# Kernel tuning notes

Measured on AMD Instinct MI355X. Metric: run time of the kernel, lower is better.

The kernel has to match this reference:

```python
import jax, jax.numpy as jnp
import numpy as np

N_NODES, N_EDGES = 50000, 800000
N_IN, E_IN, N_OUT, E_OUT = 64, 32, 64, 32


def _xavier(key, fan_in, fan_out):
    std = (2.0 / (fan_in + fan_out)) ** 0.5
    return jax.random.normal(key, (fan_in, fan_out), dtype=jnp.float32) * std


def setup_inputs() -> dict:
    key = jax.random.key(0)
    ks = jax.random.split(key, 10)
    return {
        "feat": jax.random.normal(ks[0], (N_NODES, N_IN), dtype=jnp.float32),
        "edge_feat": jax.random.normal(ks[1], (N_EDGES, E_IN), dtype=jnp.float32),
        "w_msg": _xavier(ks[2], N_IN + E_IN, N_OUT),
        "b_msg": jnp.zeros((N_OUT,), dtype=jnp.float32),
        "w_node": _xavier(ks[3], N_IN + N_OUT, N_OUT),
        "b_node": jnp.zeros((N_OUT,), dtype=jnp.float32),
        "w_edge": _xavier(ks[4], N_IN + N_OUT + E_IN, E_OUT),
        "b_edge": jnp.zeros((E_OUT,), dtype=jnp.float32),
        "src_idx": jax.random.randint(ks[5], (N_EDGES,), 0, N_NODES, dtype=jnp.int32),
        "dst_idx": jax.random.randint(ks[6], (N_EDGES,), 0, N_NODES, dtype=jnp.int32),
    }


def reference(feat, edge_feat, w_msg, b_msg, w_node, b_node, w_edge, b_edge, src_idx, dst_idx):
    n_nodes = feat.shape[0]
    # --- message: gather src + edge, linear, tanh --- [E, n_out]
    src_h = feat[src_idx]
    m = jnp.tanh(jnp.concatenate([src_h, edge_feat], axis=1) @ w_msg + b_msg)
    # --- scatter-mean into destination nodes --- [N, n_out]
    sums = jax.ops.segment_sum(m, dst_idx, num_segments=n_nodes)
    cnt = jax.ops.segment_sum(jnp.ones((m.shape[0], 1), m.dtype), dst_idx, num_segments=n_nodes)
    neigh = sums / jnp.maximum(cnt, 1.0)
    # --- node update: cat([neigh, h]) -> linear -> tanh (dropout = identity in eval) ---
    h = jnp.tanh(jnp.concatenate([neigh, feat], axis=1) @ w_node + b_node)
    # --- edge update: cat([src h, dst neigh(updated), edge h]) -> linear -> tanh ---
    e = jnp.tanh(jnp.concatenate([src_h, h[dst_idx], edge_feat], axis=1) @ w_edge + b_edge)
    return h, e
```

## Files before the change

### kernel.cpp

```cpp
#include <hip/hip_runtime.h>

#define NNODES 50000
#define NEDGES 800000
#define NPAD   50176
#define NTILE_E (NEDGES / 16)
#define NTILE_N (NNODES / 16)

typedef __attribute__((ext_vector_type(8))) short bf16x8;
typedef __attribute__((ext_vector_type(4))) float f32x4;

union ABu { bf16x8 v; uint4 u; };

__device__ __forceinline__ float fast_tanh(float x) {
    float e = __expf(2.0f * x);
    return 1.0f - 2.0f * __builtin_amdgcn_rcpf(e + 1.0f);
}

__device__ __forceinline__ unsigned pk_rne(float x, float y) {
    unsigned a = __float_as_uint(x), b = __float_as_uint(y);
    a = (a + 0x7fffu + ((a >> 16) & 1u)) >> 16;
    b = (b + 0x7fffu + ((b >> 16) & 1u)) >> 16;
    return a | (b << 16);
}
__device__ __forceinline__ unsigned pk_tr(float a, float b) {
    return __builtin_amdgcn_perm(__float_as_uint(b), __float_as_uint(a), 0x07060302);
}
__device__ __forceinline__ float bf16_lo(unsigned u) { return __uint_as_float(u << 16); }
__device__ __forceinline__ float bf16_hi(unsigned u) { return __uint_as_float(u & 0xffff0000u); }

__device__ __forceinline__ ABu make_afrag(const float* p) {
    float4 a = ((const float4*)p)[0];
    float4 b = ((const float4*)p)[1];
    ABu r;
    r.u.x = pk_tr(a.x, a.y); r.u.y = pk_tr(a.z, a.w);
    r.u.z = pk_tr(b.x, b.y); r.u.w = pk_tr(b.z, b.w);
    return r;
}

template <int LDN>
__device__ __forceinline__ ABu make_bfrag_u(const unsigned* wp) {
    ABu r;
    r.u.x = wp[0 * LDN]; r.u.y = wp[1 * LDN];
    r.u.z = wp[2 * LDN]; r.u.w = wp[3 * LDN];
    return r;
}

template <int KH, int N>
__device__ __forceinline__ void stage_w(const float* __restrict__ w, unsigned* wl_u) {
    for (int i = threadIdx.x; i < KH * N; i += 256) {
        const int kp = i / N, n = i % N;
        wl_u[i] = pk_rne(w[(2 * kp) * N + n], w[(2 * kp + 1) * N + n]);
    }
}

#define MFMA(a, b, c) __builtin_amdgcn_mfma_f32_16x16x32_bf16((a).v, (b).v, (c), 0, 0, 0)

__global__ __launch_bounds__(256) void hist_kernel(const int* __restrict__ dst_idx,
                                                   int* __restrict__ cnt,
                                                   int* __restrict__ rank) {
    const int base = (blockIdx.x * 256 + threadIdx.x) * 4;
    if (base + 4 <= NEDGES) {
        int4 d = *(const int4*)(dst_idx + base);
        int4 r;
        r.x = atomicAdd(&cnt[d.x], 1);
        r.y = atomicAdd(&cnt[d.y], 1);
        r.z = atomicAdd(&cnt[d.z], 1);
        r.w = atomicAdd(&cnt[d.w], 1);
        *(int4*)(rank + base) = r;
    }
}

__global__ __launch_bounds__(256) void scan1(const int* __restrict__ cnt,
                                             int* __restrict__ off,
                                             int* __restrict__ btot) {
    __shared__ int s[256];
    const int tid = threadIdx.x;
    const int g = blockIdx.x * 256 + tid;
    const int own = cnt[g];
    s[tid] = own;
    __syncthreads();
    for (int o = 1; o < 256; o <<= 1) {
        int v = (tid >= o) ? s[tid - o] : 0;
        __syncthreads();
        s[tid] += v;
        __syncthreads();
    }
    off[g] = s[tid] - own;
    if (tid == 255) btot[blockIdx.x] = s[255];
}

__global__ __launch_bounds__(256) void scan3b(int* __restrict__ off,
                                              const int* __restrict__ btot) {
    __shared__ int s[256];
    const int tid = threadIdx.x;
    s[tid] = btot[tid];
    __syncthreads();
    for (int o = 1; o < 256; o <<= 1) {
        int v = (tid >= o) ? s[tid - o] : 0;
        __syncthreads();
        s[tid] += v;
        __syncthreads();
    }
    const int add = (blockIdx.x == 0) ? 0 : s[blockIdx.x - 1];
    off[blockIdx.x * 256 + tid] += add;
}

__global__ __launch_bounds__(256) void rows_kernel(const int* __restrict__ dst_idx,
                                                   const int* __restrict__ off,
                                                   int* __restrict__ rank) {
    const int base = (blockIdx.x * 256 + threadIdx.x) * 4;
    if (base + 4 <= NEDGES) {
        int4 d = *(const int4*)(dst_idx + base);
        int4 r = *(const int4*)(rank + base);
        r.x += off[d.x];
        r.y += off[d.y];
        r.z += off[d.z];
        r.w += off[d.w];
        *(int4*)(rank + base) = r;
    }
}

__global__ __launch_bounds__(256) void proj2_kernel(
    const float* __restrict__ feat,
    const float* __restrict__ w_m, const float* __restrict__ b_m,
    const float* __restrict__ w_e, const float* __restrict__ b_e,
    float* __restrict__ projm, float* __restrict__ p1) {
    __shared__ __align__(16) unsigned wlm[32 * 64];
    __shared__ __align__(16) unsigned wle[32 * 32];
    stage_w<32, 64>(w_m, wlm);
    stage_w<32, 32>(w_e, wle);
    __syncthreads();

    const int lane = threadIdx.x & 63, wave = threadIdx.x >> 6;
    const int col = lane & 15, quad = lane >> 4;

    ABu bfm[2][4], bfe[2][2];
#pragma unroll
    for (int kc = 0; kc < 2; ++kc) {
#pragma unroll
        for (int nt = 0; nt < 4; ++nt)
            bfm[kc][nt] = make_bfrag_u<64>(&wlm[(kc * 16 + (quad << 2)) * 64 + nt * 16 + col]);
#pragma unroll
        for (int nt = 0; nt < 2; ++nt)
            bfe[kc][nt] = make_bfrag_u<32>(&wle[(kc * 16 + (quad << 2)) * 32 + nt * 16 + col]);
    }

    float bim[4], bie[2];
#pragma unroll
    for (int nt = 0; nt < 4; ++nt) bim[nt] = b_m[nt * 16 + col];
#pragma unroll
    for (int nt = 0; nt < 2; ++nt) bie[nt] = b_e[nt * 16 + col];

    const int nw = gridDim.x << 2;
    for (int t = (blockIdx.x << 2) + wave; t < NTILE_N; t += nw) {
        const int n0 = t << 4;
        const int n = n0 + col;
        ABu a0 = make_afrag(feat + (size_t)n * 64 + (quad << 3));
        ABu a1 = make_afrag(feat + (size_t)n * 64 + 32 + (quad << 3));

        f32x4 accm[4], acce[2];
#pragma unroll
        for (int nt = 0; nt < 4; ++nt)
            accm[nt] = (f32x4){bim[nt], bim[nt], bim[nt], bim[nt]};
#pragma unroll
        for (int nt = 0; nt < 2; ++nt)
            acce[nt] = (f32x4){bie[nt], bie[nt], bie[nt], bie[nt]};
#pragma unroll
        for (int nt = 0; nt < 4; ++nt) {
            accm[nt] = MFMA(a0, bfm[0][nt], accm[nt]);
            accm[nt] = MFMA(a1, bfm[1][nt], accm[nt]);
        }
#pragma unroll
        for (int nt = 0; nt < 2; ++nt) {
            acce[nt] = MFMA(a0, bfe[0][nt], acce[nt]);
            acce[nt] = MFMA(a1, bfe[1][nt], acce[nt]);
        }
#pragma unroll
        for (int i = 0; i < 4; ++i) {
            const int nr = n0 + (quad << 2) + i;
            float4 om = {accm[0][i], accm[1][i], accm[2][i], accm[3][i]};
            *(float4*)(projm + (size_t)nr * 64 + (col << 2)) = om;
            float2 oe = {acce[0][i], acce[1][i]};
            *(float2*)(p1 + (size_t)nr * 32 + (col << 1)) = oe;
        }
    }
}

struct MsgBuf { ABu a2; float4 f4[4]; int4 rows; };

__device__ __forceinline__ void msg_load(
    int t, int col, int quad,
    const float* __restrict__ edge_feat, const float* __restrict__ projm,
    const int* __restrict__ src_idx, const int* __restrict__ rows, MsgBuf& b) {
    const int e0 = t << 4;
    const int4 s4 = *(const int4*)(src_idx + e0 + (quad << 2));
    b.rows = *(const int4*)(rows + e0 + (quad << 2));
    b.a2 = make_afrag(edge_feat + (size_t)(e0 + col) * 32 + (quad << 3));
    b.f4[0] = *(const float4*)(projm + (size_t)s4.x * 64 + (col << 2));
    b.f4[1] = *(const float4*)(projm + (size_t)s4.y * 64 + (col << 2));
    b.f4[2] = *(const float4*)(projm + (size_t)s4.z * 64 + (col << 2));
    b.f4[3] = *(const float4*)(projm + (size_t)s4.w * 64 + (col << 2));
}

__device__ __forceinline__ void msg_comp(
    int col, const ABu (&bf)[4], const MsgBuf& b, unsigned* __restrict__ m_out) {
    f32x4 acc[4];
#pragma unroll
    for (int nt = 0; nt < 4; ++nt) acc[nt] = (f32x4){0.f, 0.f, 0.f, 0.f};
#pragma unroll
    for (int nt = 0; nt < 4; ++nt) acc[nt] = MFMA(b.a2, bf[nt], acc[nt]);
    const int rw[4] = {b.rows.x, b.rows.y, b.rows.z, b.rows.w};
#pragma unroll
    for (int i = 0; i < 4; ++i) {
        uint2 o;
        o.x = pk_rne(fast_tanh(acc[0][i] + b.f4[i].x), fast_tanh(acc[1][i] + b.f4[i].y));
        o.y = pk_rne(fast_tanh(acc[2][i] + b.f4[i].z), fast_tanh(acc[3][i] + b.f4[i].w));
        *(uint2*)(m_out + (size_t)rw[i] * 32 + (col << 1)) = o;
    }
}

__global__ __launch_bounds__(256) void msg_kernel(
    const float* __restrict__ edge_feat, const float* __restrict__ w_bot,
    const int* __restrict__ src_idx, const int* __restrict__ rows,
    const float* __restrict__ projm, unsigned* __restrict__ m_out) {
    __shared__ __align__(16) unsigned wl[16 * 64];
    stage_w<16, 64>(w_bot, wl);
    __syncthreads();

    const int lane = threadIdx.x & 63, wave = threadIdx.x >> 6;
    const int col = lane & 15, quad = lane >> 4;

    ABu bf[4];
#pragma unroll
    for (int nt = 0; nt < 4; ++nt)
        bf[nt] = make_bfrag_u<64>(&wl[(quad << 2) * 64 + nt * 16 + col]);

    const int nw = gridDim.x << 2;
    int t = (blockIdx.x << 2) + wave;
    if (t >= NTILE_E) return;
    MsgBuf A, B;
    msg_load(t, col, quad, edge_feat, projm, src_idx, rows, A);
    for (;;) {
        const int t2 = t + nw;
        if (t2 < NTILE_E)
            msg_load(t2, col, quad, edge_feat, projm, src_idx, rows, B);
        msg_comp(col, bf, A, m_out);
        if (t2 >= NTILE_E) return;
        const int t3 = t2 + nw;
        if (t3 < NTILE_E)
            msg_load(t3, col, quad, edge_feat, projm, src_idx, rows, A);
        msg_comp(col, bf, B, m_out);
        if (t3 >= NTILE_E) return;
        t = t3;
    }
}

__device__ __forceinline__ int mapk(int ks) {
    return ks < 64 ? ((ks >> 2) + ((ks >> 1) & 1) * 32 + (ks & 1) * 16) : ks;
}

__global__ __launch_bounds__(256) void gnode_kernel(
    const float* __restrict__ feat, const unsigned* __restrict__ m,
    const int* __restrict__ off, const int* __restrict__ cnt,
    const float* __restrict__ w_node, const float* __restrict__ b_node,
    const float* __restrict__ w2,
    float* __restrict__ h, float* __restrict__ p2) {
    __shared__ __align__(16) unsigned wl[64 * 64];
    __shared__ __align__(16) unsigned wl2[32 * 32];
    __shared__ float tr[4][16 * 68];

    for (int i = threadIdx.x; i < 64 * 64; i += 256) {
        const int kp = i >> 6, n = i & 63;
        wl[i] = pk_rne(w_node[mapk(2 * kp) * 64 + n], w_node[mapk(2 * kp + 1) * 64 + n]);
    }
    stage_w<32, 32>(w2, wl2);
    __syncthreads();

    const int lane = threadIdx.x & 63, wave = threadIdx.x >> 6;
    const int col = lane & 15, quad = lane >> 4;

    int t = blockIdx.x * 4 + wave;
    if (t > NTILE_N - 1) t = NTILE_N - 1;
    const int n0 = t << 4;
    const int n = n0 + col;
    const int c = cnt[n];
    const int o = off[n];

    float s0[8], s1[8];
#pragma unroll
    for (int j = 0; j < 8; ++j) { s0[j] = 0.f; s1[j] = 0.f; }
    for (int r = 0; r < c; ++r) {
        const unsigned* rp = m + (size_t)(o + r) * 32;
        const uint4 u0 = *(const uint4*)(rp + (quad << 2));
        const uint4 u1 = *(const uint4*)(rp + 16 + (quad << 2));
        s0[0] += bf16_lo(u0.x); s0[1] += bf16_hi(u0.x);
        s0[2] += bf16_lo(u0.y); s0[3] += bf16_hi(u0.y);
        s0[4] += bf16_lo(u0.z); s0[5] += bf16_hi(u0.z);
        s0[6] += bf16_lo(u0.w); s0[7] += bf16_hi(u0.w);
        s1[0] += bf16_lo(u1.x); s1[1] += bf16_hi(u1.x);
        s1[2] += bf16_lo(u1.y); s1[3] += bf16_hi(u1.y);
        s1[4] += bf16_lo(u1.z); s1[5] += bf16_hi(u1.z);
        s1[6] += bf16_lo(u1.w); s1[7] += bf16_hi(u1.w);
    }
    const float inv = __builtin_amdgcn_rcpf((float)max(c, 1));
    ABu a0, a1;
    a0.u.x = pk_tr(s0[0] * inv, s0[1] * inv); a0.u.y = pk_tr(s0[2] * inv, s0[3] * inv);
    a0.u.z = pk_tr(s0[4] * inv, s0[5] * inv); a0.u.w = pk_tr(s0[6] * inv, s0[7] * inv);
    a1.u.x = pk_tr(s1[0] * inv, s1[1] * inv); a1.u.y = pk_tr(s1[2] * inv, s1[3] * inv);
    a1.u.z = pk_tr(s1[4] * inv, s1[5] * inv); a1.u.w = pk_tr(s1[6] * inv, s1[7] * inv);
    const ABu a2 = make_afrag(feat + (size_t)n * 64 + (quad << 3));
    const ABu a3 = make_afrag(feat + (size_t)n * 64 + 32 + (quad << 3));

    f32x4 acc[4];
#pragma unroll
    for (int nt = 0; nt < 4; ++nt) {
        const float bi = b_node[nt * 16 + col];
        acc[nt] = (f32x4){bi, bi, bi, bi};
    }
#pragma unroll
    for (int nt = 0; nt < 4; ++nt) {
        acc[nt] = MFMA(a0, make_bfrag_u<64>(&wl[((quad << 2)) * 64 + nt * 16 + col]), acc[nt]);
        acc[nt] = MFMA(a1, make_bfrag_u<64>(&wl[(16 + (quad << 2)) * 64 + nt * 16 + col]), acc[nt]);
        acc[nt] = MFMA(a2, make_bfrag_u<64>(&wl[(32 + (quad << 2)) * 64 + nt * 16 + col]), acc[nt]);
        acc[nt] = MFMA(a3, make_bfrag_u<64>(&wl[(48 + (quad << 2)) * 64 + nt * 16 + col]), acc[nt]);
    }

    float* trw = tr[wave];
#pragma unroll
    for (int i = 0; i < 4; ++i) {
        const int nr = n0 + (quad << 2) + i;
#pragma unroll
        for (int nt = 0; nt < 4; ++nt) {
            const float ht = fast_tanh(acc[nt][i]);
            h[(size_t)nr * 64 + nt * 16 + col] = ht;
            trw[((quad << 2) + i) * 68 + nt * 16 + col] = ht;
        }
    }
    __syncthreads();

    float f[8], g[8];
#pragma unroll
    for (int j = 0; j < 8; ++j) {
        f[j] = trw[col * 68 + (quad << 3) + j];
        g[j] = trw[col * 68 + 32 + (quad << 3) + j];
    }
    ABu aT0, aT1;
    aT0.u.x = pk_tr(f[0], f[1]); aT0.u.y = pk_tr(f[2], f[3]);
    aT0.u.z = pk_tr(f[4], f[5]); aT0.u.w = pk_tr(f[6], f[7]);
    aT1.u.x = pk_tr(g[0], g[1]); aT1.u.y = pk_tr(g[2], g[3]);
    aT1.u.z = pk_tr(g[4], g[5]); aT1.u.w = pk_tr(g[6], g[7]);

    f32x4 acc2[2];
#pragma unroll
    for (int nt = 0; nt < 2; ++nt) acc2[nt] = (f32x4){0.f, 0.f, 0.f, 0.f};
#pragma unroll
    for (int nt = 0; nt < 2; ++nt) {
        acc2[nt] = MFMA(aT0, make_bfrag_u<32>(&wl2[((quad << 2)) * 32 + nt * 16 + col]), acc2[nt]);
        acc2[nt] = MFMA(aT1, make_bfrag_u<32>(&wl2[(16 + (quad << 2)) * 32 + nt * 16 + col]), acc2[nt]);
    }
#pragma unroll
    for (int i = 0; i < 4; ++i) {
        const int nr = n0 + (quad << 2) + i;
        float2 o2 = {acc2[0][i], acc2[1][i]};
        *(float2*)(p2 + (size_t)nr * 32 + (col << 1)) = o2;
    }
}

struct EBuf { ABu a4; float2 g1[4]; float2 g2[4]; };

__device__ __forceinline__ void edge_load(
    int t, int col, int quad,
    const float* __restrict__ edge_feat,
    const float* __restrict__ p1, const float* __restrict__ p2,
    const int* __restrict__ src_idx, const int* __restrict__ dst_idx, EBuf& b) {
    const int e0 = t << 4;
    const int4 s4 = *(const int4*)(src_idx + e0 + (quad << 2));
    const int4 d4 = *(const int4*)(dst_idx + e0 + (quad << 2));
    b.a4 = make_afrag(edge_feat + (size_t)(e0 + col) * 32 + (quad << 3));
    b.g1[0] = *(const float2*)(p1 + (size_t)s4.x * 32 + (col << 1));
    b.g1[1] = *(const float2*)(p1 + (size_t)s4.y * 32 + (col << 1));
    b.g1[2] = *(const float2*)(p1 + (size_t)s4.z * 32 + (col << 1));
    b.g1[3] = *(const float2*)(p1 + (size_t)s4.w * 32 + (col << 1));
    b.g2[0] = *(const float2*)(p2 + (size_t)d4.x * 32 + (col << 1));
    b.g2[1] = *(const float2*)(p2 + (size_t)d4.y * 32 + (col << 1));
    b.g2[2] = *(const float2*)(p2 + (size_t)d4.z * 32 + (col << 1));
    b.g2[3] = *(const float2*)(p2 + (size_t)d4.w * 32 + (col << 1));
}

__device__ __forceinline__ void edge_comp(
    int t, int col, int quad, const ABu (&bf)[2],
    const EBuf& b, float* __restrict__ e_out) {
    f32x4 acc[2];
#pragma unroll
    for (int nt = 0; nt < 2; ++nt) acc[nt] = (f32x4){0.f, 0.f, 0.f, 0.f};
#pragma unroll
    for (int nt = 0; nt < 2; ++nt) acc[nt] = MFMA(b.a4, bf[nt], acc[nt]);
    const int e0 = t << 4;
#pragma unroll
    for (int i = 0; i < 4; ++i) {
        const int er = e0 + (quad << 2) + i;
        e_out[(size_t)er * 32 + col] = fast_tanh(acc[0][i] + b.g1[i].x + b.g2[i].x);
        e_out[(size_t)er * 32 + 16 + col] = fast_tanh(acc[1][i] + b.g1[i].y + b.g2[i].y);
    }
}

__global__ __launch_bounds__(256) void edge_update(
    const float* __restrict__ edge_feat, const float* __restrict__ w3,
    const float* __restrict__ p1, const float* __restrict__ p2,
    const int* __restrict__ src_idx, const int* __restrict__ dst_idx,
    float* __restrict__ e_out) {
    __shared__ __align__(16) unsigned wl[16 * 32];
    stage_w<16, 32>(w3, wl);
    __syncthreads();

    const int lane = threadIdx.x & 63, wave = threadIdx.x >> 6;
    const int col = lane & 15, quad = lane >> 4;

    ABu bf[2];
#pragma unroll
    for (int nt = 0; nt < 2; ++nt)
        bf[nt] = make_bfrag_u<32>(&wl[(quad << 2) * 32 + nt * 16 + col]);

    const int nw = gridDim.x << 2;
    int t = (blockIdx.x << 2) + wave;
    if (t >= NTILE_E) return;
    EBuf A, B;
    edge_load(t, col, quad, edge_feat, p1, p2, src_idx, dst_idx, A);
    for (;;) {
        const int t2 = t + nw;
        if (t2 < NTILE_E)
            edge_load(t2, col, quad, edge_feat, p1, p2, src_idx, dst_idx, B);
        edge_comp(t, col, quad, bf, A, e_out);
        if (t2 >= NTILE_E) return;
        const int t3 = t2 + nw;
        if (t3 < NTILE_E)
            edge_load(t3, col, quad, edge_feat, p1, p2, src_idx, dst_idx, A);
        edge_comp(t2, col, quad, bf, B, e_out);
        if (t3 >= NTILE_E) return;
        t = t3;
    }
}

extern "C" void kernel_launch(void* const* d_in, const int* in_sizes, int n_in,
                              void* d_out, int out_size, void* d_ws, size_t ws_size,
                              hipStream_t stream) {
    const float* feat      = (const float*)d_in[0];
    const float* edge_feat = (const float*)d_in[1];
    const float* w_msg     = (const float*)d_in[2];
    const float* b_msg     = (const float*)d_in[3];
    const float* w_node    = (const float*)d_in[4];
    const float* b_node    = (const float*)d_in[5];
    const float* w_edge    = (const float*)d_in[6];
    const float* b_edge    = (const float*)d_in[7];
    const int*   src_idx   = (const int*)d_in[8];
    const int*   dst_idx   = (const int*)d_in[9];

    float* h = (float*)d_out;
    float* e = (float*)d_out + (size_t)NNODES * 64;
    unsigned* m = (unsigned*)e;
    float* projm = h;

    int* cnt  = (int*)d_ws;
    int* off  = cnt + NPAD;
    int* btot = off + NPAD;
    int* rank = btot + 256;
    float* p1 = (float*)(rank + NEDGES);
    float* p2 = p1 + (size_t)NNODES * 32;

    hipMemsetAsync(cnt, 0, NPAD * sizeof(int), stream);
    hipMemsetAsync(btot, 0, 256 * sizeof(int), stream);

    hist_kernel<<<(NEDGES / 4 + 255) / 256, 256, 0, stream>>>(dst_idx, cnt, rank);
    scan1<<<NPAD / 256, 256, 0, stream>>>(cnt, off, btot);
    scan3b<<<NPAD / 256, 256, 0, stream>>>(off, btot);
    rows_kernel<<<(NEDGES / 4 + 255) / 256, 256, 0, stream>>>(dst_idx, off, rank);
    proj2_kernel<<<256, 256, 0, stream>>>(feat, w_msg, b_msg, w_edge, b_edge, projm, p1);
    msg_kernel<<<2500, 256, 0, stream>>>(edge_feat, w_msg + 64 * 64,
                                         src_idx, rank, projm, m);
    gnode_kernel<<<(NTILE_N + 3) / 4, 256, 0, stream>>>(feat, m, off, cnt,
                                                        w_node, b_node,
                                                        w_edge + 64 * 32, h, p2);
    edge_update<<<2500, 256, 0, stream>>>(edge_feat, w_edge + 128 * 32,
                                          p1, p2, src_idx, dst_idx, e);
}
```

Measured before the change: 379.4 us.

## Merge histogram with projection kernel and restructure neighbor aggregation in node kernel

Folds the dst histogram atomics and the node projection GEMM into one launch, splitting work by block index, and drops the btot memset by guarding the scan read. The node kernel now aggregates messages with all 64 lanes cooperating per node, using cross-quad shuffles and staging the mean through shared memory, where before each lane looped serially over its own node's edges. The A-fragment for the second GEMM is read straight from shared memory instead of being transposed through scalar loads. Together these cut launch count and give more even, coalesced parallelism in the gather, in exchange for an extra block barrier and a serial per-node loop inside each wave.

```diff
diff --git a/kernel.cpp b/kernel.cpp
--- a/kernel.cpp
+++ b/kernel.cpp
@@ -5,6 +5,7 @@
 #define NPAD   50176
 #define NTILE_E (NEDGES / 16)
 #define NTILE_N (NNODES / 16)
+#define HIST_BLOCKS 782
 
 typedef __attribute__((ext_vector_type(8))) short bf16x8;
 typedef __attribute__((ext_vector_type(4))) float f32x4;
@@ -55,18 +56,86 @@
 
 #define MFMA(a, b, c) __builtin_amdgcn_mfma_f32_16x16x32_bf16((a).v, (b).v, (c), 0, 0, 0)
 
-__global__ __launch_bounds__(256) void hist_kernel(const int* __restrict__ dst_idx,
-                                                   int* __restrict__ cnt,
-                                                   int* __restrict__ rank) {
-    const int base = (blockIdx.x * 256 + threadIdx.x) * 4;
-    if (base + 4 <= NEDGES) {
-        int4 d = *(const int4*)(dst_idx + base);
-        int4 r;
-        r.x = atomicAdd(&cnt[d.x], 1);
-        r.y = atomicAdd(&cnt[d.y], 1);
-        r.z = atomicAdd(&cnt[d.z], 1);
-        r.w = atomicAdd(&cnt[d.w], 1);
-        *(int4*)(rank + base) = r;
+__global__ __launch_bounds__(256) void hist_proj2(
+    const int* __restrict__ dst_idx, int* __restrict__ cnt, int* __restrict__ rank,
+    const float* __restrict__ feat,
+    const float* __restrict__ w_m, const float* __restrict__ b_m,
+    const float* __restrict__ w_e, const float* __restrict__ b_e,
+    float* __restrict__ projm, float* __restrict__ p1) {
+    __shared__ __align__(16) unsigned wlm[32 * 64];
+    __shared__ __align__(16) unsigned wle[32 * 32];
+
+    if (blockIdx.x < HIST_BLOCKS) {
+        const int base = (blockIdx.x * 256 + threadIdx.x) * 4;
+        if (base + 4 <= NEDGES) {
+            int4 d = *(const int4*)(dst_idx + base);
+            int4 r;
+            r.x = atomicAdd(&cnt[d.x], 1);
+            r.y = atomicAdd(&cnt[d.y], 1);
+            r.z = atomicAdd(&cnt[d.z], 1);
+            r.w = atomicAdd(&cnt[d.w], 1);
+            *(int4*)(rank + base) = r;
+        }
+        return;
+    }
+
+    const int pb = blockIdx.x - HIST_BLOCKS;
+    stage_w<32, 64>(w_m, wlm);
+    stage_w<32, 32>(w_e, wle);
+    __syncthreads();
+
+    const int lane = threadIdx.x & 63, wave = threadIdx.x >> 6;
+    const int col = lane & 15, quad = lane >> 4;
+
+    ABu bfm[2][4], bfe[2][2];
+#pragma unroll
+    for (int kc = 0; kc < 2; ++kc) {
+#pragma unroll
+        for (int nt = 0; nt < 4; ++nt)
+            bfm[kc][nt] = make_bfrag_u<64>(&wlm[(kc * 16 + (quad << 2)) * 64 + nt * 16 + col]);
+#pragma unroll
+        for (int nt = 0; nt < 2; ++nt)
+            bfe[kc][nt] = make_bfrag_u<32>(&wle[(kc * 16 + (quad << 2)) * 32 + nt * 16 + col]);
+    }
+
+    float bim[4], bie[2];
+#pragma unroll
+    for (int nt = 0; nt < 4; ++nt) bim[nt] = b_m[nt * 16 + col];
+#pragma unroll
+    for (int nt = 0; nt < 2; ++nt) bie[nt] = b_e[nt * 16 + col];
+
+    const int nw = 256 << 2;
+    for (int t = (pb << 2) + wave; t < NTILE_N; t += nw) {
+        const int n0 = t << 4;
+        const int n = n0 + col;
+        ABu a0 = make_afrag(feat + (size_t)n * 64 + (quad << 3));
+        ABu a1 = make_afrag(feat + (size_t)n * 64 + 32 + (quad << 3));
+
+        f32x4 accm[4], acce[2];
+#pragma unroll
+        for (int nt = 0; nt < 4; ++nt)
+            accm[nt] = (f32x4){bim[nt], bim[nt], bim[nt], bim[nt]};
+#pragma unroll
+        for (int nt = 0; nt < 2; ++nt)
+            acce[nt] = (f32x4){bie[nt], bie[nt], bie[nt], bie[nt]};
+#pragma unroll
+        for (int nt = 0; nt < 4; ++nt) {
+            accm[nt] = MFMA(a0, bfm[0][nt], accm[nt]);
+            accm[nt] = MFMA(a1, bfm[1][nt], accm[nt]);
+        }
+#pragma unroll
+        for (int nt = 0; nt < 2; ++nt) {
+            acce[nt] = MFMA(a0, bfe[0][nt], acce[nt]);
+            acce[nt] = MFMA(a1, bfe[1][nt], acce[nt]);
+        }
+#pragma unroll
+        for (int i = 0; i < 4; ++i) {
+            const int nr = n0 + (quad << 2) + i;
+            float4 om = {accm[0][i], accm[1][i], accm[2][i], accm[3][i]};
+            *(float4*)(projm + (size_t)nr * 64 + (col << 2)) = om;
+            float2 oe = {acce[0][i], acce[1][i]};
+            *(float2*)(p1 + (size_t)nr * 32 + (col << 1)) = oe;
+        }
     }
 }
 
@@ -93,7 +162,7 @@
                                               const int* __restrict__ btot) {
     __shared__ int s[256];
     const int tid = threadIdx.x;
-    s[tid] = btot[tid];
+    s[tid] = (tid < NPAD / 256) ? btot[tid] : 0;
     __syncthreads();
     for (int o = 1; o < 256; o <<= 1) {
         int v = (tid >= o) ? s[tid - o] : 0;
@@ -117,72 +186,6 @@
         r.z += off[d.z];
         r.w += off[d.w];
         *(int4*)(rank + base) = r;
-    }
-}
-
-__global__ __launch_bounds__(256) void proj2_kernel(
-    const float* __restrict__ feat,
-    const float* __restrict__ w_m, const float* __restrict__ b_m,
-    const float* __restrict__ w_e, const float* __restrict__ b_e,
-    float* __restrict__ projm, float* __restrict__ p1) {
-    __shared__ __align__(16) unsigned wlm[32 * 64];
-    __shared__ __align__(16) unsigned wle[32 * 32];
-    stage_w<32, 64>(w_m, wlm);
-    stage_w<32, 32>(w_e, wle);
-    __syncthreads();
-
-    const int lane = threadIdx.x & 63, wave = threadIdx.x >> 6;
-    const int col = lane & 15, quad = lane >> 4;
-
-    ABu bfm[2][4], bfe[2][2];
-#pragma unroll
-    for (int kc = 0; kc < 2; ++kc) {
-#pragma unroll
-        for (int nt = 0; nt < 4; ++nt)
-            bfm[kc][nt] = make_bfrag_u<64>(&wlm[(kc * 16 + (quad << 2)) * 64 + nt * 16 + col]);
-#pragma unroll
-        for (int nt = 0; nt < 2; ++nt)
-            bfe[kc][nt] = make_bfrag_u<32>(&wle[(kc * 16 + (quad << 2)) * 32 + nt * 16 + col]);
-    }
-
-    float bim[4], bie[2];
-#pragma unroll
-    for (int nt = 0; nt < 4; ++nt) bim[nt] = b_m[nt * 16 + col];
-#pragma unroll
-    for (int nt = 0; nt < 2; ++nt) bie[nt] = b_e[nt * 16 + col];
-
-    const int nw = gridDim.x << 2;
-    for (int t = (blockIdx.x << 2) + wave; t < NTILE_N; t += nw) {
-        const int n0 = t << 4;
-        const int n = n0 + col;
-        ABu a0 = make_afrag(feat + (size_t)n * 64 + (quad << 3));
-        ABu a1 = make_afrag(feat + (size_t)n * 64 + 32 + (quad << 3));
-
-        f32x4 accm[4], acce[2];
-#pragma unroll
-        for (int nt = 0; nt < 4; ++nt)
-            accm[nt] = (f32x4){bim[nt], bim[nt], bim[nt], bim[nt]};
-#pragma unroll
-        for (int nt = 0; nt < 2; ++nt)
-            acce[nt] = (f32x4){bie[nt], bie[nt], bie[nt], bie[nt]};
-#pragma unroll
-        for (int nt = 0; nt < 4; ++nt) {
-            accm[nt] = MFMA(a0, bfm[0][nt], accm[nt]);
-            accm[nt] = MFMA(a1, bfm[1][nt], accm[nt]);
-        }
-#pragma unroll
-        for (int nt = 0; nt < 2; ++nt) {
-            acce[nt] = MFMA(a0, bfe[0][nt], acce[nt]);
-            acce[nt] = MFMA(a1, bfe[1][nt], acce[nt]);
-        }
-#pragma unroll
-        for (int i = 0; i < 4; ++i) {
-            const int nr = n0 + (quad << 2) + i;
-            float4 om = {accm[0][i], accm[1][i], accm[2][i], accm[3][i]};
-            *(float4*)(projm + (size_t)nr * 64 + (col << 2)) = om;
-            float2 oe = {acce[0][i], acce[1][i]};
-            *(float2*)(p1 + (size_t)nr * 32 + (col << 1)) = oe;
-        }
     }
 }
 
@@ -261,13 +264,13 @@
 
 __global__ __launch_bounds__(256) void gnode_kernel(
     const float* __restrict__ feat, const unsigned* __restrict__ m,
-    const int* __restrict__ off, const int* __restrict__ cnt,
+    const int* __restrict__ off,
     const float* __restrict__ w_node, const float* __restrict__ b_node,
     const float* __restrict__ w2,
     float* __restrict__ h, float* __restrict__ p2) {
     __shared__ __align__(16) unsigned wl[64 * 64];
     __shared__ __align__(16) unsigned wl2[32 * 32];
-    __shared__ float tr[4][16 * 68];
+    __shared__ __align__(16) float as[4][16 * 68];
 
     for (int i = threadIdx.x; i < 64 * 64; i += 256) {
         const int kp = i >> 6, n = i & 63;
@@ -282,32 +285,35 @@
     int t = blockIdx.x * 4 + wave;
     if (t > NTILE_N - 1) t = NTILE_N - 1;
     const int n0 = t << 4;
+    float* asw = as[wave];
+
+    int obase = off[n0];
+    for (int node = 0; node < 16; ++node) {
+        const int onext = off[n0 + node + 1];
+        const int c = onext - obase;
+        float s0 = 0.f, s1 = 0.f, s2 = 0.f, s3 = 0.f;
+        for (int r = quad; r < c; r += 4) {
+            const uint2 u = *(const uint2*)(m + (size_t)(obase + r) * 32 + (col << 1));
+            s0 += bf16_lo(u.x); s1 += bf16_hi(u.x);
+            s2 += bf16_lo(u.y); s3 += bf16_hi(u.y);
+        }
+        s0 += __shfl_xor(s0, 16); s1 += __shfl_xor(s1, 16);
+        s2 += __shfl_xor(s2, 16); s3 += __shfl_xor(s3, 16);
+        s0 += __shfl_xor(s0, 32); s1 += __shfl_xor(s1, 32);
+        s2 += __shfl_xor(s2, 32); s3 += __shfl_xor(s3, 32);
+        if (quad == 0) {
+            const float inv = __builtin_amdgcn_rcpf((float)max(c, 1));
+            float4 o4 = {s0 * inv, s1 * inv, s2 * inv, s3 * inv};
+            *(float4*)(asw + node * 68 + (col << 2)) = o4;
+        }
+        obase = onext;
+    }
+    __syncthreads();
+
+    const float* ac = asw + col * 68;
+    const ABu a0 = make_afrag(ac + (quad << 3));
+    const ABu a1 = make_afrag(ac + 32 + (quad << 3));
     const int n = n0 + col;
-    const int c = cnt[n];
-    const int o = off[n];
-
-    float s0[8], s1[8];
-#pragma unroll
-    for (int j = 0; j < 8; ++j) { s0[j] = 0.f; s1[j] = 0.f; }
-    for (int r = 0; r < c; ++r) {
-        const unsigned* rp = m + (size_t)(o + r) * 32;
-        const uint4 u0 = *(const uint4*)(rp + (quad << 2));
-        const uint4 u1 = *(const uint4*)(rp + 16 + (quad << 2));
-        s0[0] += bf16_lo(u0.x); s0[1] += bf16_hi(u0.x);
-        s0[2] += bf16_lo(u0.y); s0[3] += bf16_hi(u0.y);
-        s0[4] += bf16_lo(u0.z); s0[5] += bf16_hi(u0.z);
-        s0[6] += bf16_lo(u0.w); s0[7] += bf16_hi(u0.w);
-        s1[0] += bf16_lo(u1.x); s1[1] += bf16_hi(u1.x);
-        s1[2] += bf16_lo(u1.y); s1[3] += bf16_hi(u1.y);
-        s1[4] += bf16_lo(u1.z); s1[5] += bf16_hi(u1.z);
-        s1[6] += bf16_lo(u1.w); s1[7] += bf16_hi(u1.w);
-    }
-    const float inv = __builtin_amdgcn_rcpf((float)max(c, 1));
-    ABu a0, a1;
-    a0.u.x = pk_tr(s0[0] * inv, s0[1] * inv); a0.u.y = pk_tr(s0[2] * inv, s0[3] * inv);
-    a0.u.z = pk_tr(s0[4] * inv, s0[5] * inv); a0.u.w = pk_tr(s0[6] * inv, s0[7] * inv);
-    a1.u.x = pk_tr(s1[0] * inv, s1[1] * inv); a1.u.y = pk_tr(s1[2] * inv, s1[3] * inv);
-    a1.u.z = pk_tr(s1[4] * inv, s1[5] * inv); a1.u.w = pk_tr(s1[6] * inv, s1[7] * inv);
     const ABu a2 = make_afrag(feat + (size_t)n * 64 + (quad << 3));
     const ABu a3 = make_afrag(feat + (size_t)n * 64 + 32 + (quad << 3));
 
@@ -324,8 +330,8 @@
         acc[nt] = MFMA(a2, make_bfrag_u<64>(&wl[(32 + (quad << 2)) * 64 + nt * 16 + col]), acc[nt]);
         acc[nt] = MFMA(a3, make_bfrag_u<64>(&wl[(48 + (quad << 2)) * 64 + nt * 16 + col]), acc[nt]);
     }
-
-    float* trw = tr[wave];
+    __syncthreads();
+
 #pragma unroll
     for (int i = 0; i < 4; ++i) {
         const int nr = n0 + (quad << 2) + i;
@@ -333,22 +339,14 @@
         for (int nt = 0; nt < 4; ++nt) {
             const float ht = fast_tanh(acc[nt][i]);
             h[(size_t)nr * 64 + nt * 16 + col] = ht;
-            trw[((quad << 2) + i) * 68 + nt * 16 + col] = ht;
-        }
-    }
-    __syncthreads();
-
-    float f[8], g[8];
-#pragma unroll
-    for (int j = 0; j < 8; ++j) {
-        f[j] = trw[col * 68 + (quad << 3) + j];
-        g[j] = trw[col * 68 + 32 + (quad << 3) + j];
-    }
-    ABu aT0, aT1;
-    aT0.u.x = pk_tr(f[0], f[1]); aT0.u.y = pk_tr(f[2], f[3]);
-    aT0.u.z = pk_tr(f[4], f[5]); aT0.u.w = pk_tr(f[6], f[7]);
-    aT1.u.x = pk_tr(g[0], g[1]); aT1.u.y = pk_tr(g[2], g[3]);
-    aT1.u.z = pk_tr(g[4], g[5]); aT1.u.w = pk_tr(g[6], g[7]);
+            asw[((quad << 2) + i) * 68 + nt * 16 + col] = ht;
+        }
+    }
+    __syncthreads();
+
+    const float* tc = asw + col * 68;
+    ABu aT0 = make_afrag(tc + (quad << 3));
+    ABu aT1 = make_afrag(tc + 32 + (quad << 3));
 
     f32x4 acc2[2];
 #pragma unroll
@@ -468,16 +466,16 @@
     float* p2 = p1 + (size_t)NNODES * 32;
 
     hipMemsetAsync(cnt, 0, NPAD * sizeof(int), stream);
-    hipMemsetAsync(btot, 0, 256 * sizeof(int), stream);
-
-    hist_kernel<<<(NEDGES / 4 + 255) / 256, 256, 0, stream>>>(dst_idx, cnt, rank);
+
+    hist_proj2<<<HIST_BLOCKS + 256, 256, 0, stream>>>(dst_idx, cnt, rank, feat,
+                                                      w_msg, b_msg, w_edge, b_edge,
+                                                      projm, p1);
     scan1<<<NPAD / 256, 256, 0, stream>>>(cnt, off, btot);
     scan3b<<<NPAD / 256, 256, 0, stream>>>(off, btot);
-    rows_kernel<<<(NEDGES / 4 + 255) / 256, 256, 0, stream>>>(dst_idx, off, rank);
-    proj2_kernel<<<256, 256, 0, stream>>>(feat, w_msg, b_msg, w_edge, b_edge, projm, p1);
+    rows_kernel<<<HIST_BLOCKS, 256, 0, stream>>>(dst_idx, off, rank);
     msg_kernel<<<2500, 256, 0, stream>>>(edge_feat, w_msg + 64 * 64,
                                          src_idx, rank, projm, m);
-    gnode_kernel<<<(NTILE_N + 3) / 4, 256, 0, stream>>>(feat, m, off, cnt,
+    gnode_kernel<<<(NTILE_N + 3) / 4, 256, 0, stream>>>(feat, m, off,
                                                         w_node, b_node,
                                                         w_edge + 64 * 32, h, p2);
     edge_update<<<2500, 256, 0, stream>>>(edge_feat, w_edge + 128 * 32,
```

Result: no change. 383.2 us (+1.0%).
